# Performance work log

Hardware: AMD Instinct MI355X
Metric: run time of the kernel (lower is better)

The kernel has to match this reference:

```python
import jax, jax.numpy as jnp
import numpy as np

B, T, IDIM, ODIM, HDIM, CDIM = 8, 8192, 256, 256, 1024, 128


def setup_inputs() -> dict:
    key = jax.random.key(0)
    ks = jax.random.split(key, 7)
    s_enc = 1.0 / np.sqrt(IDIM)
    s_dec = 1.0 / np.sqrt(HDIM)
    return {
        "x": jax.random.normal(ks[0], (B, T, IDIM), jnp.float32),
        "mask_prev": jnp.zeros((B, T, HDIM), jnp.float32),
        "W_enc": jax.random.uniform(ks[1], (IDIM, HDIM), jnp.float32, -s_enc, s_enc),
        "b_enc": jax.random.uniform(ks[2], (HDIM,), jnp.float32, -s_enc, s_enc),
        "W_dec_self": jax.random.uniform(ks[3], (HDIM, IDIM), jnp.float32, -s_dec, s_dec),
        "b_dec_self": jax.random.uniform(ks[4], (IDIM,), jnp.float32, -s_dec, s_dec),
        "W_dec_src": jax.random.uniform(ks[5], (HDIM, ODIM), jnp.float32, -s_dec, s_dec),
        "b_dec_src": jax.random.uniform(ks[6], (ODIM,), jnp.float32, -s_dec, s_dec),
        "decoder_type": 0,  # 0 = 'self', 1 = 'src'
    }


def _topk_masks(h, cdim):
    # energy_pooling_mask with share=True: topk(k=2*cdim) of h^2 along hdim.
    energy = h * h  # [B,T,H]
    _, idx = jax.lax.top_k(energy, 2 * cdim)  # [B,T,2C] indices into H
    bi = jnp.arange(h.shape[0])[:, None, None]
    ti = jnp.arange(h.shape[1])[None, :, None]
    # scatter instead of materializing one_hot [B,T,2C,H]
    mask = jnp.zeros_like(h).at[bi, ti, idx[..., :cdim]].add(1.0)
    mask_share = jnp.zeros_like(h).at[bi, ti, idx].add(1.0)
    return mask, mask_share


def reference(x, mask_prev, W_enc, b_enc, W_dec_self, b_dec_self, W_dec_src, b_dec_src, decoder_type):
    # encoder
    h = jnp.einsum("bti,ih->bth", x, W_enc) + b_enc  # [B,T,H]
    # hidden_exclude_activation (mask_prev provided): zero previously-used units
    h = jnp.where(mask_prev > 0, 0.0, h)
    mask_cur, mask_cur_share = _topk_masks(h, CDIM)
    mask_new = mask_prev + mask_cur
    h = jnp.where(mask_cur_share > 0, h, 0.0)
    # decoder (idim == odim asserted in original)
    if decoder_type == 0:
        out = jnp.einsum("bth,ho->bto", h, W_dec_self) + b_dec_self
    else:
        out = jnp.einsum("bth,ho->bto", h, W_dec_src) + b_dec_src
    return out, mask_new
```

## Files before the change

### kernel.cpp

```cpp
#include <hip/hip_runtime.h>
#include <hip/hip_bf16.h>

#define B_ 8
#define T_ 8192
#define M_ (B_ * T_)
#define IDIM 256
#define HDIM 1024
#define ODIM 256
#define CDIM 128
#define OUT_OFF ((size_t)M_ * ODIM)

typedef __attribute__((ext_vector_type(4))) float floatx4;
typedef __attribute__((ext_vector_type(8))) short shortx8;

__global__ __launch_bounds__(256) void k0_convw(const float* __restrict__ Wself,
                                                const float* __restrict__ Wsrc,
                                                const int* __restrict__ dtype,
                                                __hip_bfloat16* __restrict__ WdT) {
    int id = blockIdx.x * 256 + threadIdx.x;
    int n = id >> 10;
    int k = id & 1023;
    const float* W = (*dtype == 0) ? Wself : Wsrc;
    WdT[id] = __float2bfloat16(W[(size_t)k * ODIM + n]);
}

__global__ __launch_bounds__(256) void k1_enc(const float* __restrict__ X,
                                              const float* __restrict__ W,
                                              const float* __restrict__ bias,
                                              float* __restrict__ H) {
    __shared__ __align__(16) float As[32][128];
    __shared__ __align__(16) float Bs[32][128];
    const int t  = threadIdx.x;
    const int m0 = blockIdx.x * 128;
    const int n0 = blockIdx.y * 128;
    const int tx = t & 15;
    const int ty = t >> 4;

    float acc[8][8];
#pragma unroll
    for (int i = 0; i < 8; ++i)
#pragma unroll
        for (int j = 0; j < 8; ++j) acc[i][j] = 0.0f;

    for (int kk = 0; kk < IDIM; kk += 32) {
#pragma unroll
        for (int r = 0; r < 4; ++r) {
            int idx = t + r * 256;
            int row = idx >> 3;
            int k4  = (idx & 7) << 2;
            float4 a = *(const float4*)(X + (size_t)(m0 + row) * IDIM + kk + k4);
            int col = row ^ k4;
            As[k4 + 0][col] = a.x;
            As[k4 + 1][col] = a.y;
            As[k4 + 2][col] = a.z;
            As[k4 + 3][col] = a.w;
        }
#pragma unroll
        for (int r = 0; r < 4; ++r) {
            int idx = t + r * 256;
            int row = idx >> 5;
            int c4  = (idx & 31) << 2;
            *(float4*)&Bs[row][c4] =
                *(const float4*)(W + (size_t)(kk + row) * HDIM + n0 + c4);
        }
        __syncthreads();

#pragma unroll 8
        for (int k = 0; k < 32; ++k) {
            const int s = k & 28;
            float4 a0 = *(const float4*)&As[k][(ty * 8) ^ s];
            float4 a1 = *(const float4*)&As[k][(ty * 8 + 4) ^ s];
            float4 b0 = *(const float4*)&Bs[k][tx * 4];
            float4 b1 = *(const float4*)&Bs[k][tx * 4 + 64];
            float av[8] = {a0.x, a0.y, a0.z, a0.w, a1.x, a1.y, a1.z, a1.w};
            float bv[8] = {b0.x, b0.y, b0.z, b0.w, b1.x, b1.y, b1.z, b1.w};
#pragma unroll
            for (int i = 0; i < 8; ++i)
#pragma unroll
                for (int j = 0; j < 8; ++j)
                    acc[i][j] = fmaf(av[i], bv[j], acc[i][j]);
        }
        __syncthreads();
    }

#pragma unroll
    for (int i = 0; i < 8; ++i) {
        int gm = m0 + ty * 8 + i;
        float* o = H + (size_t)gm * HDIM + n0;
        float4 v0, v1;
        v0.x = acc[i][0] + bias[n0 + tx * 4 + 0];
        v0.y = acc[i][1] + bias[n0 + tx * 4 + 1];
        v0.z = acc[i][2] + bias[n0 + tx * 4 + 2];
        v0.w = acc[i][3] + bias[n0 + tx * 4 + 3];
        v1.x = acc[i][4] + bias[n0 + 64 + tx * 4 + 0];
        v1.y = acc[i][5] + bias[n0 + 64 + tx * 4 + 1];
        v1.z = acc[i][6] + bias[n0 + 64 + tx * 4 + 2];
        v1.w = acc[i][7] + bias[n0 + 64 + tx * 4 + 3];
        *(float4*)(o + tx * 4) = v0;
        *(float4*)(o + 64 + tx * 4) = v1;
    }
}

#define NBIN 512
#define KBASE 1600
#define CAP 128

__device__ __forceinline__ unsigned int bsearch_kth(const unsigned int* u, int k,
                                                    int lane, int* r_out) {
    unsigned long long lo = 0, hi = 0xFFFFFFFFull;
    while (lo < hi) {
        unsigned int mid = (unsigned int)((lo + hi + 1) >> 1);
        int c = 0;
#pragma unroll
        for (int i = 0; i < 16; ++i) c += (u[i] >= mid) ? 1 : 0;
#pragma unroll
        for (int off = 1; off < 64; off <<= 1) {
            int o = __shfl_down(c, off, 64);
            if (lane + off < 64) c += o;
        }
        c = __shfl(c, 0);
        if (c >= k) lo = mid; else hi = (unsigned long long)mid - 1;
    }
    unsigned int T = (unsigned int)lo;
    int g = 0;
#pragma unroll
    for (int i = 0; i < 16; ++i) g += (u[i] > T) ? 1 : 0;
#pragma unroll
    for (int off = 1; off < 64; off <<= 1) {
        int o = __shfl_down(g, off, 64);
        if (lane + off < 64) g += o;
    }
    g = __shfl(g, 0);
    *r_out = k - g;
    return T;
}

__global__ __launch_bounds__(256) void k2_topk(const float* __restrict__ mask_prev,
                                               float* __restrict__ Hio,
                                               __hip_bfloat16* __restrict__ Abf) {
    __shared__ unsigned int hist[4][NBIN];
    __shared__ unsigned long long cand[4][2][CAP];
    __shared__ unsigned int sres[4][8];
    __shared__ unsigned int scnt[4][2];
    const int t = threadIdx.x;
    const int wave = t >> 6;
    const int lane = t & 63;
    const size_t row = (size_t)blockIdx.x * 4 + wave;
    const float* mp = mask_prev + row * HDIM + lane * 16;
    float* hrow = Hio + row * HDIM + lane * 16;

    float hv[16], mpv[16];
    unsigned int u[16];
    int bin[16];
#pragma unroll
    for (int c = 0; c < 4; ++c) {
        float4 m4 = *(const float4*)(mp + c * 4);
        float4 h4 = *(const float4*)(hrow + c * 4);
        float mm[4] = {m4.x, m4.y, m4.z, m4.w};
        float hh[4] = {h4.x, h4.y, h4.z, h4.w};
#pragma unroll
        for (int x = 0; x < 4; ++x) {
            int i = c * 4 + x;
            float h = (mm[x] > 0.0f) ? 0.0f : hh[x];
            mpv[i] = mm[x]; hv[i] = h;
            u[i] = __float_as_uint(h * h);
            int b = (int)(u[i] >> 19) - KBASE;
            bin[i] = (b < 0) ? 0 : ((b > NBIN - 1) ? NBIN - 1 : b);
        }
    }

#pragma unroll
    for (int q = 0; q < 8; ++q) hist[wave][lane + (q << 6)] = 0u;
    if (lane < 2) scnt[wave][lane] = 0u;
    __syncthreads();
#pragma unroll
    for (int i = 0; i < 16; ++i) atomicAdd(&hist[wave][bin[i]], 1u);
    __syncthreads();

    {
        unsigned int cj[8]; unsigned int lt = 0;
#pragma unroll
        for (int jj = 0; jj < 8; ++jj) { cj[jj] = hist[wave][lane * 8 + jj]; lt += cj[jj]; }
        unsigned int s = lt;
#pragma unroll
        for (int off = 1; off < 64; off <<= 1) {
            unsigned int o = (unsigned int)__shfl_down((int)s, off, 64);
            if (lane + off < 64) s += o;
        }
        unsigned int run = s - lt;
#pragma unroll
        for (int jj = 7; jj >= 0; --jj) {
            unsigned int gt = run, ge = run + cj[jj];
            if (gt < CDIM && CDIM <= ge)         { sres[wave][0] = lane * 8 + jj; sres[wave][1] = CDIM - gt; }
            if (gt < 2 * CDIM && 2 * CDIM <= ge) { sres[wave][2] = lane * 8 + jj; sres[wave][3] = 2 * CDIM - gt; }
            run = ge;
        }
    }
    __syncthreads();
    const unsigned int b1 = sres[wave][0], kk1 = sres[wave][1];
    const unsigned int b2 = sres[wave][2], kk2 = sres[wave][3];

#pragma unroll
    for (int i = 0; i < 16; ++i) {
        int j = lane * 16 + i;
        unsigned long long pk = ((unsigned long long)u[i] << 32) | (unsigned int)(1023 - j);
        if ((unsigned int)bin[i] == b1) {
            unsigned int p = atomicAdd(&scnt[wave][0], 1u);
            if (p < CAP) cand[wave][0][p] = pk;
        }
        if (b2 != b1 && (unsigned int)bin[i] == b2) {
            unsigned int p = atomicAdd(&scnt[wave][1], 1u);
            if (p < CAP) cand[wave][1][p] = pk;
        }
    }
    __syncthreads();
    const unsigned int C1 = scnt[wave][0];
    const unsigned int C2 = (b2 == b1) ? C1 : scnt[wave][1];
    const unsigned long long* L2 = (b2 == b1) ? cand[wave][0] : cand[wave][1];

    if (C1 <= CAP) {
        for (unsigned int idx = lane; idx < C1; idx += 64) {
            unsigned long long mine = cand[wave][0][idx];
            unsigned int myu = (unsigned int)(mine >> 32);
            unsigned int rank = 0, gtu = 0;
            for (unsigned int c = 0; c < C1; ++c) {
                unsigned long long o = cand[wave][0][c];
                rank += (o > mine) ? 1u : 0u;
                gtu  += ((unsigned int)(o >> 32) > myu) ? 1u : 0u;
            }
            if (rank == kk1 - 1) { sres[wave][4] = myu; sres[wave][5] = gtu; }
        }
    }
    if (C2 <= CAP) {
        for (unsigned int idx = lane; idx < C2; idx += 64) {
            unsigned long long mine = L2[idx];
            unsigned int myu = (unsigned int)(mine >> 32);
            unsigned int rank = 0, gtu = 0;
            for (unsigned int c = 0; c < C2; ++c) {
                unsigned long long o = L2[c];
                rank += (o > mine) ? 1u : 0u;
                gtu  += ((unsigned int)(o >> 32) > myu) ? 1u : 0u;
            }
            if (rank == kk2 - 1) { sres[wave][6] = myu; sres[wave][7] = gtu; }
        }
    }
    __syncthreads();

    unsigned int T1, T2; int r1, r2;
    if (C1 <= CAP) { T1 = sres[wave][4]; r1 = (int)(kk1 - sres[wave][5]); }
    else           { T1 = bsearch_kth(u, CDIM, lane, &r1); }
    if (C2 <= CAP) { T2 = sres[wave][6]; r2 = (int)(kk2 - sres[wave][7]); }
    else           { T2 = bsearch_kth(u, 2 * CDIM, lane, &r2); }

    int p1[16], p2[16];
    int tot1 = 0, tot2 = 0;
#pragma unroll
    for (int i = 0; i < 16; ++i) {
        p1[i] = tot1; p2[i] = tot2;
        tot1 += (u[i] == T1) ? 1 : 0;
        tot2 += (u[i] == T2) ? 1 : 0;
    }
    int s1v = tot1, s2v = tot2;
#pragma unroll
    for (int off = 1; off < 64; off <<= 1) {
        int o1 = __shfl_up(s1v, off, 64);
        int o2 = __shfl_up(s2v, off, 64);
        if (lane >= off) { s1v += o1; s2v += o2; }
    }
    const int ex1 = s1v - tot1;
    const int ex2 = s2v - tot2;

#pragma unroll
    for (int c = 0; c < 4; ++c) {
        float v[4];
#pragma unroll
        for (int x = 0; x < 4; ++x) {
            int i = c * 4 + x;
            bool s1 = (u[i] > T1) || ((u[i] == T1) && (ex1 + p1[i] < r1));
            v[x] = mpv[i] + (s1 ? 1.0f : 0.0f);
        }
        float4 v4 = {v[0], v[1], v[2], v[3]};
        *(float4*)(hrow + c * 4) = v4;
    }
    __hip_bfloat16* ab = Abf + row * HDIM + lane * 16;
#pragma unroll
    for (int half = 0; half < 2; ++half) {
        union { unsigned short us[8]; uint4 v; } pk;
#pragma unroll
        for (int x = 0; x < 8; ++x) {
            int i = half * 8 + x;
            bool s2 = (u[i] > T2) || ((u[i] == T2) && (ex2 + p2[i] < r2));
            __hip_bfloat16 bb = __float2bfloat16(s2 ? hv[i] : 0.0f);
            pk.us[x] = *(unsigned short*)&bb;
        }
        *(uint4*)(ab + half * 8) = pk.v;
    }
}

#define K3LD 40
__global__ __launch_bounds__(256) void k3_dec(const __hip_bfloat16* __restrict__ A,
                                              const __hip_bfloat16* __restrict__ Bt,
                                              const float* __restrict__ bias_self,
                                              const float* __restrict__ bias_src,
                                              const int* __restrict__ dtype,
                                              float* __restrict__ Out) {
    __shared__ __align__(16) __hip_bfloat16 As[128 * K3LD];
    __shared__ __align__(16) __hip_bfloat16 Bs[128 * K3LD];
    const int t = threadIdx.x;
    const int lane = t & 63;
    const int wave = t >> 6;
    const int m0 = blockIdx.x * 128;
    const int n0 = blockIdx.y * 128;
    const int wr = wave >> 1;
    const int wc = wave & 1;
    const int quad = lane >> 4;
    const int rf = lane & 15;

    int srow[2], skc[2];
#pragma unroll
    for (int p = 0; p < 2; ++p) {
        int l = p * 256 + t;
        srow[p] = l >> 2;
        skc[p]  = (l & 3) << 3;
    }

    floatx4 acc[4][4];
    const floatx4 z = {0.0f, 0.0f, 0.0f, 0.0f};
#pragma unroll
    for (int i = 0; i < 4; ++i)
#pragma unroll
        for (int j = 0; j < 4; ++j) acc[i][j] = z;

    uint4 apre[2], bpre[2];
#pragma unroll
    for (int p = 0; p < 2; ++p) {
        apre[p] = *(const uint4*)(A  + (size_t)(m0 + srow[p]) * HDIM + skc[p]);
        bpre[p] = *(const uint4*)(Bt + (size_t)(n0 + srow[p]) * HDIM + skc[p]);
    }
#pragma unroll
    for (int p = 0; p < 2; ++p) {
        *(uint4*)&As[srow[p] * K3LD + skc[p]] = apre[p];
        *(uint4*)&Bs[srow[p] * K3LD + skc[p]] = bpre[p];
    }
    __syncthreads();

#pragma unroll 1
    for (int kt = 0; kt < HDIM / 32; ++kt) {
        if (kt < HDIM / 32 - 1) {
            int kn = (kt + 1) * 32;
#pragma unroll
            for (int p = 0; p < 2; ++p) {
                apre[p] = *(const uint4*)(A  + (size_t)(m0 + srow[p]) * HDIM + kn + skc[p]);
                bpre[p] = *(const uint4*)(Bt + (size_t)(n0 + srow[p]) * HDIM + kn + skc[p]);
            }
        }
        shortx8 af[4], bf[4];
#pragma unroll
        for (int i = 0; i < 4; ++i) {
            af[i] = *(const shortx8*)&As[(wr * 64 + i * 16 + rf) * K3LD + quad * 8];
            bf[i] = *(const shortx8*)&Bs[(wc * 64 + i * 16 + rf) * K3LD + quad * 8];
        }
#pragma unroll
        for (int mi = 0; mi < 4; ++mi)
#pragma unroll
            for (int nj = 0; nj < 4; ++nj)
                acc[mi][nj] = __builtin_amdgcn_mfma_f32_16x16x32_bf16(
                    af[mi], bf[nj], acc[mi][nj], 0, 0, 0);
        __syncthreads();
        if (kt < HDIM / 32 - 1) {
#pragma unroll
            for (int p = 0; p < 2; ++p) {
                *(uint4*)&As[srow[p] * K3LD + skc[p]] = apre[p];
                *(uint4*)&Bs[srow[p] * K3LD + skc[p]] = bpre[p];
            }
            __syncthreads();
        }
    }

    const float* bias = (*dtype == 0) ? bias_self : bias_src;
#pragma unroll
    for (int mi = 0; mi < 4; ++mi) {
#pragma unroll
        for (int nj = 0; nj < 4; ++nj) {
            int gn = n0 + wc * 64 + nj * 16 + rf;
            float bv = bias[gn];
            int gmb = m0 + wr * 64 + mi * 16 + quad * 4;
#pragma unroll
            for (int r2 = 0; r2 < 4; ++r2)
                Out[(size_t)(gmb + r2) * ODIM + gn] = acc[mi][nj][r2] + bv;
        }
    }
}

extern "C" void kernel_launch(void* const* d_in, const int* in_sizes, int n_in,
                              void* d_out, int out_size, void* d_ws, size_t ws_size,
                              hipStream_t stream) {
    const float* x          = (const float*)d_in[0];
    const float* mask_prev  = (const float*)d_in[1];
    const float* W_enc      = (const float*)d_in[2];
    const float* b_enc      = (const float*)d_in[3];
    const float* W_dec_self = (const float*)d_in[4];
    const float* b_dec_self = (const float*)d_in[5];
    const float* W_dec_src  = (const float*)d_in[6];
    const float* b_dec_src  = (const float*)d_in[7];
    const int*   dtype      = (const int*)d_in[8];

    float* out  = (float*)d_out;
    float* Hbuf = out + OUT_OFF;

    __hip_bfloat16* Abf = (__hip_bfloat16*)d_ws;
    __hip_bfloat16* WdT = (__hip_bfloat16*)((char*)d_ws + (size_t)M_ * HDIM * 2);

    k0_convw<<<dim3((ODIM * HDIM) / 256), 256, 0, stream>>>(W_dec_self, W_dec_src, dtype, WdT);
    const size_t half = (size_t)(M_ / 2);
    k1_enc<<<dim3(M_ / 256, HDIM / 128), 256, 0, stream>>>(x, W_enc, b_enc, Hbuf);
    k1_enc<<<dim3(M_ / 256, HDIM / 128), 256, 0, stream>>>(x + half * IDIM, W_enc, b_enc,
                                                           Hbuf + half * HDIM);
    k2_topk <<<dim3(M_ / 4), 256, 0, stream>>>(mask_prev, Hbuf, Abf);
    k3_dec  <<<dim3(M_ / 128, ODIM / 128), 256, 0, stream>>>(Abf, WdT, b_dec_self, b_dec_src, dtype, out);
}
```

Before: 1.158 ms.

## Double-buffer encoder GEMM B tiles with direct global-to-LDS loads and prefetch

The FP32 encoder GEMM now prefetches the next K-tile while computing the current one. The W tile is double-buffered in LDS and loaded with global_load_lds, and the X tile is staged through registers and transposed into LDS after compute. Address arithmetic is hoisted out of the loop, occupancy is hinted with launch_bounds(256,3), and the two half-size launches are merged into one. This aims to hide global memory latency behind FMA work, at the cost of more LDS, more registers and an extra barrier per iteration.

Result: no change. 1.165 ms (+0.6%).

```diff
diff --git a/kernel.cpp b/kernel.cpp
--- a/kernel.cpp
+++ b/kernel.cpp
@@ -12,6 +12,12 @@
 
 typedef __attribute__((ext_vector_type(4))) float floatx4;
 typedef __attribute__((ext_vector_type(8))) short shortx8;
+
+__device__ __forceinline__ void glds16(const float* g, void* lds) {
+    __builtin_amdgcn_global_load_lds(
+        (const __attribute__((address_space(1))) void*)g,
+        (__attribute__((address_space(3))) void*)lds, 16, 0, 0);
+}
 
 __global__ __launch_bounds__(256) void k0_convw(const float* __restrict__ Wself,
                                                 const float* __restrict__ Wsrc,
@@ -24,17 +30,38 @@
     WdT[id] = __float2bfloat16(W[(size_t)k * ODIM + n]);
 }
 
-__global__ __launch_bounds__(256) void k1_enc(const float* __restrict__ X,
-                                              const float* __restrict__ W,
-                                              const float* __restrict__ bias,
-                                              float* __restrict__ H) {
+__global__ __launch_bounds__(256, 3) void k1_enc(const float* __restrict__ X,
+                                                 const float* __restrict__ W,
+                                                 const float* __restrict__ bias,
+                                                 float* __restrict__ H) {
     __shared__ __align__(16) float As[32][128];
-    __shared__ __align__(16) float Bs[32][128];
+    __shared__ __align__(16) float Bs[2][32][128];
     const int t  = threadIdx.x;
     const int m0 = blockIdx.x * 128;
     const int n0 = blockIdx.y * 128;
     const int tx = t & 15;
     const int ty = t >> 4;
+    const int wavebase = t & ~63;
+
+    int acol[4], ak4[4];
+    const float* aptr[4];
+#pragma unroll
+    for (int r = 0; r < 4; ++r) {
+        int idx = r * 256 + t;
+        int row = idx >> 3;
+        int k4  = (idx & 7) << 2;
+        ak4[r]  = k4;
+        acol[r] = row ^ k4;
+        aptr[r] = X + (size_t)(m0 + row) * IDIM + k4;
+    }
+    const float* bptr[4];
+#pragma unroll
+    for (int r = 0; r < 4; ++r) {
+        int idx = r * 256 + t;
+        int row = idx >> 5;
+        int c4  = (idx & 31) << 2;
+        bptr[r] = W + (size_t)row * HDIM + n0 + c4;
+    }
 
     float acc[8][8];
 #pragma unroll
@@ -42,36 +69,43 @@
 #pragma unroll
         for (int j = 0; j < 8; ++j) acc[i][j] = 0.0f;
 
-    for (int kk = 0; kk < IDIM; kk += 32) {
-#pragma unroll
-        for (int r = 0; r < 4; ++r) {
-            int idx = t + r * 256;
-            int row = idx >> 3;
-            int k4  = (idx & 7) << 2;
-            float4 a = *(const float4*)(X + (size_t)(m0 + row) * IDIM + kk + k4);
-            int col = row ^ k4;
-            As[k4 + 0][col] = a.x;
-            As[k4 + 1][col] = a.y;
-            As[k4 + 2][col] = a.z;
-            As[k4 + 3][col] = a.w;
-        }
-#pragma unroll
-        for (int r = 0; r < 4; ++r) {
-            int idx = t + r * 256;
-            int row = idx >> 5;
-            int c4  = (idx & 31) << 2;
-            *(float4*)&Bs[row][c4] =
-                *(const float4*)(W + (size_t)(kk + row) * HDIM + n0 + c4);
-        }
-        __syncthreads();
+    float4 areg[4];
+
+#pragma unroll
+    for (int r = 0; r < 4; ++r) areg[r] = *(const float4*)(aptr[r]);
+#pragma unroll
+    for (int r = 0; r < 4; ++r)
+        glds16(bptr[r], (char*)&Bs[0][0][0] + (size_t)(r * 256 + wavebase) * 16);
+#pragma unroll
+    for (int r = 0; r < 4; ++r) {
+        As[ak4[r] + 0][acol[r]] = areg[r].x;
+        As[ak4[r] + 1][acol[r]] = areg[r].y;
+        As[ak4[r] + 2][acol[r]] = areg[r].z;
+        As[ak4[r] + 3][acol[r]] = areg[r].w;
+    }
+    asm volatile("s_waitcnt vmcnt(0)");
+    __syncthreads();
+
+#pragma unroll 1
+    for (int tt = 0; tt < IDIM / 32; ++tt) {
+        const int cur = tt & 1;
+        if (tt < IDIM / 32 - 1) {
+            const int kn = (tt + 1) * 32;
+#pragma unroll
+            for (int r = 0; r < 4; ++r)
+                glds16(bptr[r] + (size_t)kn * HDIM,
+                       (char*)&Bs[cur ^ 1][0][0] + (size_t)(r * 256 + wavebase) * 16);
+#pragma unroll
+            for (int r = 0; r < 4; ++r) areg[r] = *(const float4*)(aptr[r] + kn);
+        }
 
 #pragma unroll 8
         for (int k = 0; k < 32; ++k) {
             const int s = k & 28;
             float4 a0 = *(const float4*)&As[k][(ty * 8) ^ s];
             float4 a1 = *(const float4*)&As[k][(ty * 8 + 4) ^ s];
-            float4 b0 = *(const float4*)&Bs[k][tx * 4];
-            float4 b1 = *(const float4*)&Bs[k][tx * 4 + 64];
+            float4 b0 = *(const float4*)&Bs[cur][k][tx * 4];
+            float4 b1 = *(const float4*)&Bs[cur][k][tx * 4 + 64];
             float av[8] = {a0.x, a0.y, a0.z, a0.w, a1.x, a1.y, a1.z, a1.w};
             float bv[8] = {b0.x, b0.y, b0.z, b0.w, b1.x, b1.y, b1.z, b1.w};
 #pragma unroll
@@ -80,7 +114,19 @@
                 for (int j = 0; j < 8; ++j)
                     acc[i][j] = fmaf(av[i], bv[j], acc[i][j]);
         }
-        __syncthreads();
+
+        if (tt < IDIM / 32 - 1) {
+            asm volatile("s_waitcnt vmcnt(0)");
+            __syncthreads();
+#pragma unroll
+            for (int r = 0; r < 4; ++r) {
+                As[ak4[r] + 0][acol[r]] = areg[r].x;
+                As[ak4[r] + 1][acol[r]] = areg[r].y;
+                As[ak4[r] + 2][acol[r]] = areg[r].z;
+                As[ak4[r] + 3][acol[r]] = areg[r].w;
+            }
+            __syncthreads();
+        }
     }
 
 #pragma unroll
@@ -412,10 +458,7 @@
     __hip_bfloat16* WdT = (__hip_bfloat16*)((char*)d_ws + (size_t)M_ * HDIM * 2);
 
     k0_convw<<<dim3((ODIM * HDIM) / 256), 256, 0, stream>>>(W_dec_self, W_dec_src, dtype, WdT);
-    const size_t half = (size_t)(M_ / 2);
-    k1_enc<<<dim3(M_ / 256, HDIM / 128), 256, 0, stream>>>(x, W_enc, b_enc, Hbuf);
-    k1_enc<<<dim3(M_ / 256, HDIM / 128), 256, 0, stream>>>(x + half * IDIM, W_enc, b_enc,
-                                                           Hbuf + half * HDIM);
+    k1_enc  <<<dim3(M_ / 128, HDIM / 128), 256, 0, stream>>>(x, W_enc, b_enc, Hbuf);
     k2_topk <<<dim3(M_ / 4), 256, 0, stream>>>(mask_prev, Hbuf, Abf);
     k3_dec  <<<dim3(M_ / 128, ODIM / 128), 256, 0, stream>>>(Abf, WdT, b_dec_self, b_dec_src, dtype, out);
 }
```
